# Performance work log

Hardware: AMD Instinct MI355X
Metric: run time of the kernel (lower is better)

## Reference

```python
import math
import jax, jax.numpy as jnp
import numpy as np

EMBED_DIM = 1024
NUM_HEADS = 16
HEAD_DIM = EMBED_DIM // NUM_HEADS


def setup_inputs() -> dict:
    key = jax.random.key(0)
    kx, kqkv, kproj = jax.random.split(key, 3)
    b, sq, h = 2, 2048, EMBED_DIM
    x = jax.random.normal(kx, (b, sq, h), dtype=jnp.float32)
    # torch Linear weights are [out_features, in_features]
    # xavier_uniform for qkv: bound = sqrt(6/(fan_in+fan_out))
    bound_qkv = math.sqrt(6.0 / (h + 3 * h))
    Wqkv = jax.random.uniform(kqkv, (3 * h, h), dtype=jnp.float32,
                              minval=-bound_qkv, maxval=bound_qkv)
    # kaiming_uniform(a=sqrt(5)) for proj: bound = 1/sqrt(fan_in)
    bound_p = 1.0 / math.sqrt(h)
    Wproj = jax.random.uniform(kproj, (h, h), dtype=jnp.float32,
                               minval=-bound_p, maxval=bound_p)
    bproj = jnp.zeros((h,), dtype=jnp.float32)
    # self-attention: query == key == value (module asserts equality)
    return {"query": x, "key": x, "value": x,
            "Wqkv": Wqkv, "Wproj": Wproj, "bproj": bproj}


def reference(query, key, value, Wqkv, Wproj, bproj):
    b, sq, h = query.shape
    nh, hn = NUM_HEADS, HEAD_DIM
    # permute to [sq, b, h] then flatten tokens (seq-major)
    x = jnp.transpose(query, (1, 0, 2)).reshape(sq * b, h)
    qkv = x @ Wqkv.T                       # [sq*b, 3h] (no qkv bias: add_bias_kv=False)
    qkv = qkv.reshape(sq, b, nh, 3 * hn)
    q, k, v = jnp.split(qkv, 3, axis=-1)   # each [sq, b, nh, hn]
    # view to (sq, b*nh, hn) then transpose(0,1) -> [b*nh, sq, hn] (b-major, nh-minor)
    q = q.reshape(sq, b * nh, hn).transpose(1, 0, 2)
    k = k.reshape(sq, b * nh, hn).transpose(1, 0, 2)
    v = v.reshape(sq, b * nh, hn).transpose(1, 0, 2)
    scale = 1.0 / math.sqrt(hn)
    scores = jnp.einsum('nqd,nkd->nqk', q, k) * scale   # [b*nh, sq, sq] full matrix
    attn = jax.nn.softmax(scores, axis=-1)
    ctx = jnp.einsum('nqk,nkd->nqd', attn, v)           # [b*nh, sq, hn]
    # NOTE: original code views the b*nh (b-major) dim as (nh, b) -- reproduce exactly
    ctx = ctx.reshape(nh, b, sq, hn)
    ctx = jnp.transpose(ctx, (2, 1, 0, 3)).reshape(sq * b, h)
    out = ctx @ Wproj.T + bproj
    out = out.reshape(sq, b, h)
    return jnp.transpose(out, (1, 0, 2))   # [b, sq, h]
```

## Files before the change

### kernel.cpp

```cpp
#include <hip/hip_runtime.h>
#include <stdint.h>

#define B_   2
#define SQ   2048
#define H    1024
#define NH   16
#define HN   64
#define T_TOK 4096
#define N3H  3072

typedef __bf16 bf16x8 __attribute__((ext_vector_type(8)));
typedef float  f32x4  __attribute__((ext_vector_type(4)));

#define MFMA16(a, b, c) __builtin_amdgcn_mfma_f32_16x16x32_bf16((a), (b), (c), 0, 0, 0)

#define LGKM_DRAIN() do { \
  __builtin_amdgcn_s_waitcnt(0xC07F); \
  __builtin_amdgcn_wave_barrier(); \
} while (0)

__device__ __forceinline__ uint16_t f2bf_u(float f) {
  union { float f; uint32_t u; } v; v.f = f;
  uint32_t u = v.u;
  u += 0x7fffu + ((u >> 16) & 1u);
  return (uint16_t)(u >> 16);
}

__device__ __forceinline__ bf16x8 ldb8(const uint16_t* p) {
  return *reinterpret_cast<const bf16x8*>(p);
}

__device__ __forceinline__ void gll16(const uint16_t* g, uint16_t* l) {
  __builtin_amdgcn_global_load_lds(
      (const __attribute__((address_space(1))) uint32_t*)g,
      (__attribute__((address_space(3))) uint32_t*)l, 16, 0, 0);
}

__global__ __launch_bounds__(256) void convert_kernel(
    const float* __restrict__ x, const float* __restrict__ wqkv,
    const float* __restrict__ wproj,
    uint16_t* __restrict__ xb, uint16_t* __restrict__ wqkvb,
    uint16_t* __restrict__ wprojb) {
  const int XT4 = (T_TOK * H) / 4;
  const int WQ4 = (N3H * H) / 4;
  int i4 = blockIdx.x * 256 + threadIdx.x;
  const float* src;
  uint16_t* dst;
  if (i4 < XT4) {
    int i = i4 * 4;
    int t = i >> 10, c = i & 1023;
    int bi = t & 1, s = t >> 1;
    src = x + (bi * SQ + s) * H + c;
    dst = xb + i;
  } else if (i4 < XT4 + WQ4) {
    int j = (i4 - XT4) * 4;
    src = wqkv + j; dst = wqkvb + j;
  } else {
    int j = (i4 - XT4 - WQ4) * 4;
    src = wproj + j; dst = wprojb + j;
  }
  float4 v = *(const float4*)src;
  ushort4 o;
  o.x = f2bf_u(v.x); o.y = f2bf_u(v.y); o.z = f2bf_u(v.z); o.w = f2bf_u(v.w);
  *(ushort4*)dst = o;
}

__global__ __launch_bounds__(256) void gemm_qkv_kernel(
    const uint16_t* __restrict__ xb, const uint16_t* __restrict__ wb,
    uint16_t* __restrict__ Qb, uint16_t* __restrict__ Kb,
    uint16_t* __restrict__ Vtb) {
  const int lane = threadIdx.x & 63;
  const int wave = threadIdx.x >> 6;
  const int quad = lane >> 4, l16 = lane & 15;
  const int wm = wave >> 1, wn = wave & 1;
  const int row0 = blockIdx.y * 128, col0 = blockIdx.x * 128;

  __shared__ __align__(16) char smem[4 * 64 * 76 * 2];
  uint16_t* sA = (uint16_t*)smem;
  uint16_t* sB = (uint16_t*)(smem + 8192);
  uint16_t* W  = (uint16_t*)(smem) + wave * (64 * 76);

  const int lrow = lane >> 2;
  const int lk   = (lane & 3) * 8;

  f32x4 acc[4][4];
#pragma unroll
  for (int i = 0; i < 4; ++i)
#pragma unroll
    for (int j = 0; j < 4; ++j) acc[i][j] = (f32x4){0.f, 0.f, 0.f, 0.f};

  for (int k0 = 0; k0 < H; k0 += 32) {
#pragma unroll
    for (int c = 0; c < 2; ++c) {
      int g = c * 4 + wave;
      gll16(xb + (size_t)(row0 + g * 16 + lrow) * H + k0 + lk, sA + g * 512);
      gll16(wb + (size_t)(col0 + g * 16 + lrow) * H + k0 + lk, sB + g * 512);
    }
    __syncthreads();
    bf16x8 af[4], bfr[4];
#pragma unroll
    for (int mt = 0; mt < 4; ++mt)
      af[mt] = ldb8(sA + (wm * 64 + mt * 16 + l16) * 32 + quad * 8);
#pragma unroll
    for (int nt = 0; nt < 4; ++nt)
      bfr[nt] = ldb8(sB + (wn * 64 + nt * 16 + l16) * 32 + quad * 8);
#pragma unroll
    for (int mt = 0; mt < 4; ++mt)
#pragma unroll
      for (int nt = 0; nt < 4; ++nt)
        acc[mt][nt] = MFMA16(af[mt], bfr[nt], acc[mt][nt]);
    __syncthreads();
  }

  const int c0 = col0 + wn * 64;
  const int cm = c0 >> 6;
  const int hd = cm / 3;
  const int which = cm - hd * 3;
  const int t0 = row0 + wm * 64;

  if (which < 2) {
#pragma unroll
    for (int mt = 0; mt < 4; ++mt)
#pragma unroll
      for (int nt = 0; nt < 4; ++nt)
#pragma unroll
        for (int r = 0; r < 4; ++r)
          W[(mt * 16 + quad * 4 + r) * 76 + nt * 16 + l16] = f2bf_u(acc[mt][nt][r]);
    LGKM_DRAIN();
    uint16_t* dstb = (which == 0) ? Qb : Kb;
    const int t8 = lane >> 3, d0 = (lane & 7) * 8;
#pragma unroll
    for (int it = 0; it < 8; ++it) {
      int tl = it * 8 + t8;
      int t = t0 + tl;
      int s = t >> 1;
      int n = (t & 1) * NH + hd;
      bf16x8 vv = ldb8(W + tl * 76 + d0);
      *(bf16x8*)(dstb + (size_t)(n * SQ + s) * HN + d0) = vv;
    }
  } else {
    uint32_t* W32 = (uint32_t*)W;
#pragma unroll
    for (int mt = 0; mt < 4; ++mt)
#pragma unroll
      for (int nt = 0; nt < 4; ++nt) {
        int base = (nt * 16 + l16) * 76 + mt * 8 + quad * 2;
        W32[base >> 1] =
            (uint32_t)f2bf_u(acc[mt][nt][0]) | ((uint32_t)f2bf_u(acc[mt][nt][2]) << 16);
        W32[(base >> 1) + 16] =
            (uint32_t)f2bf_u(acc[mt][nt][1]) | ((uint32_t)f2bf_u(acc[mt][nt][3]) << 16);
      }
    LGKM_DRAIN();
    const int dl = lane >> 3;
    const int bi = (lane >> 2) & 1;
    const int sc = (lane & 3) * 8;
    const int s0 = (row0 >> 1) + wm * 32;
    const int n = bi * NH + hd;
#pragma unroll
    for (int it = 0; it < 8; ++it) {
      int d = it * 8 + dl;
      bf16x8 vv = ldb8(W + d * 76 + bi * 32 + sc);
      *(bf16x8*)(Vtb + (size_t)(n * HN + d) * SQ + s0 + sc) = vv;
    }
  }
}

__global__ __launch_bounds__(512, 6) void attn_kernel(
    const uint16_t* __restrict__ Qb, const uint16_t* __restrict__ Kb,
    const uint16_t* __restrict__ Vtb, uint16_t* __restrict__ ctxb) {
  const int lane = threadIdx.x & 63;
  const int wave = threadIdx.x >> 6;
  const int quad = lane >> 4, l16 = lane & 15;
  const int head  = blockIdx.x;
  const int qtile = blockIdx.y;
  const int wq = wave & 3;
  const int hf = wave >> 2;
  const int q0 = qtile * 64 + wq * 16;

  const uint16_t* Qh = Qb + (size_t)head * SQ * HN;
  const uint16_t* Kh = Kb + (size_t)head * SQ * HN;
  const uint16_t* Vh = Vtb + (size_t)head * HN * SQ;

  __shared__ __align__(16) char smem_raw[51200];
  uint16_t (*stage)[2][64][64] = (uint16_t(*)[2][64][64])smem_raw;
  float (*cacc)[64][21]        = (float(*)[64][21])smem_raw;
  uint16_t (*plds)[16][72]     = (uint16_t(*)[16][72])(smem_raw + 32768);

  const int lr8 = lane >> 3;
  const int lc8 = lane & 7;
  const int sc8 = (lc8 - lr8) & 7;

  bf16x8 aq0 = ldb8(Qh + (q0 + l16) * HN + quad * 8);
  bf16x8 aq1 = ldb8(Qh + (q0 + l16) * HN + 32 + quad * 8);

  float lrun[4];
  f32x4 acc[4];
#pragma unroll
  for (int r = 0; r < 4; ++r) {
    lrun[r] = 0.f;
    acc[r] = (f32x4){0.f, 0.f, 0.f, 0.f};
  }
  const float sc2 = 0.125f * 1.44269504f;

  for (int kt = 0; kt < 16; ++kt) {
    const int kbase = (hf * 16 + kt) * 64;
#pragma unroll
    for (int j = 0; j < 2; ++j) {
      int rr = wq * 16 + j * 8;
      gll16(Kh + (size_t)(kbase + rr + lr8) * HN + sc8 * 8, &stage[hf][0][rr][0]);
      gll16(Vh + (size_t)(rr + lr8) * SQ + kbase + sc8 * 8, &stage[hf][1][rr][0]);
    }
    __syncthreads();

    f32x4 s4[4];
#pragma unroll
    for (int st = 0; st < 4; ++st) {
      bf16x8 k0 = ldb8(&stage[hf][0][st * 16 + l16][0] + ((quad + l16) & 7) * 8);
      bf16x8 k1 = ldb8(&stage[hf][0][st * 16 + l16][0] + ((quad + 4 + l16) & 7) * 8);
      f32x4 z = (f32x4){0.f, 0.f, 0.f, 0.f};
      z = MFMA16(aq0, k0, z);
      s4[st] = MFMA16(aq1, k1, z);
    }
#pragma unroll
    for (int st = 0; st < 4; ++st)
#pragma unroll
      for (int r = 0; r < 4; ++r) {
        float p = __builtin_amdgcn_exp2f(s4[st][r] * sc2);
        plds[wave][quad * 4 + r][st * 16 + l16] = f2bf_u(p);
        lrun[r] += p;
      }
    LGKM_DRAIN();
    bf16x8 ap0 = ldb8(&plds[wave][l16][quad * 8]);
    bf16x8 ap1 = ldb8(&plds[wave][l16][32 + quad * 8]);
#pragma unroll
    for (int dt = 0; dt < 4; ++dt) {
      bf16x8 v0 = ldb8(&stage[hf][1][dt * 16 + l16][0] + ((quad + l16) & 7) * 8);
      bf16x8 v1 = ldb8(&stage[hf][1][dt * 16 + l16][0] + ((quad + 4 + l16) & 7) * 8);
      acc[dt] = MFMA16(ap0, v0, acc[dt]);
      acc[dt] = MFMA16(ap1, v1, acc[dt]);
    }
    __syncthreads();
  }

  if (hf) {
    float* dst = cacc[wq][lane];
#pragma unroll
    for (int dt = 0; dt < 4; ++dt)
#pragma unroll
      for (int r = 0; r < 4; ++r) dst[dt * 4 + r] = acc[dt][r];
#pragma unroll
    for (int r = 0; r < 4; ++r) dst[16 + r] = lrun[r];
  }
  __syncthreads();
  if (hf) return;
  {
    const float* src = cacc[wq][lane];
#pragma unroll
    for (int dt = 0; dt < 4; ++dt)
#pragma unroll
      for (int r = 0; r < 4; ++r) acc[dt][r] += src[dt * 4 + r];
#pragma unroll
    for (int r = 0; r < 4; ++r) lrun[r] += src[16 + r];
  }

  float rinv[4];
#pragma unroll
  for (int r = 0; r < 4; ++r) {
    float ls = lrun[r];
    ls += __shfl_xor(ls, 1);
    ls += __shfl_xor(ls, 2);
    ls += __shfl_xor(ls, 4);
    ls += __shfl_xor(ls, 8);
    rinv[r] = __builtin_amdgcn_rcpf(ls);
  }
#pragma unroll
  for (int dt = 0; dt < 4; ++dt)
#pragma unroll
    for (int r = 0; r < 4; ++r)
      plds[wave][quad * 4 + r][dt * 16 + l16] = f2bf_u(acc[dt][r] * rinv[r]);
  LGKM_DRAIN();
  {
    const int q8 = lane >> 3, d0 = (lane & 7) * 8;
    const int gc = (head >> 1) * HN + d0;
#pragma unroll
    for (int it = 0; it < 2; ++it) {
      int ql = it * 8 + q8;
      bf16x8 vv = ldb8(&plds[wave][ql][d0]);
      int row = 2 * (q0 + ql) + (head & 1);
      *(bf16x8*)(ctxb + (size_t)row * H + gc) = vv;
    }
  }
}

__global__ __launch_bounds__(256) void gemm_proj_kernel(
    const uint16_t* __restrict__ ab, const uint16_t* __restrict__ wb,
    const float* __restrict__ bias, float* __restrict__ out) {
  const int lane = threadIdx.x & 63;
  const int wave = threadIdx.x >> 6;
  const int quad = lane >> 4, l16 = lane & 15;
  const int row0 = blockIdx.y * 128, col0 = blockIdx.x * 64;

  __shared__ __align__(16) uint16_t sA[128 * 32];
  __shared__ __align__(16) uint16_t sB[64 * 32];

  const int lrow = lane >> 2;
  const int lk   = (lane & 3) * 8;

  f32x4 acc[2][4];
#pragma unroll
  for (int i = 0; i < 2; ++i)
#pragma unroll
    for (int j = 0; j < 4; ++j) acc[i][j] = (f32x4){0.f, 0.f, 0.f, 0.f};

  for (int k0 = 0; k0 < H; k0 += 32) {
#pragma unroll
    for (int c = 0; c < 2; ++c) {
      int g = c * 4 + wave;
      gll16(ab + (size_t)(row0 + g * 16 + lrow) * H + k0 + lk, sA + g * 512);
    }
    gll16(wb + (size_t)(col0 + wave * 16 + lrow) * H + k0 + lk, sB + wave * 512);
    __syncthreads();
    bf16x8 af[2], bfr[4];
#pragma unroll
    for (int mt = 0; mt < 2; ++mt)
      af[mt] = ldb8(sA + (wave * 32 + mt * 16 + l16) * 32 + quad * 8);
#pragma unroll
    for (int nt = 0; nt < 4; ++nt)
      bfr[nt] = ldb8(sB + (nt * 16 + l16) * 32 + quad * 8);
#pragma unroll
    for (int mt = 0; mt < 2; ++mt)
#pragma unroll
      for (int nt = 0; nt < 4; ++nt)
        acc[mt][nt] = MFMA16(af[mt], bfr[nt], acc[mt][nt]);
    __syncthreads();
  }

#pragma unroll
  for (int mt = 0; mt < 2; ++mt)
#pragma unroll
    for (int nt = 0; nt < 4; ++nt)
#pragma unroll
      for (int r = 0; r < 4; ++r) {
        int m = row0 + wave * 32 + mt * 16 + quad * 4 + r;
        int c = col0 + nt * 16 + l16;
        int s = m >> 1, bi = m & 1;
        out[(size_t)(bi * SQ + s) * H + c] = acc[mt][nt][r] + bias[c];
      }
}

extern "C" void kernel_launch(void* const* d_in, const int* in_sizes, int n_in,
                              void* d_out, int out_size, void* d_ws, size_t ws_size,
                              hipStream_t stream) {
  const float* x     = (const float*)d_in[0];
  const float* wqkv  = (const float*)d_in[3];
  const float* wproj = (const float*)d_in[4];
  const float* bproj = (const float*)d_in[5];
  float* out = (float*)d_out;

  char* ws = (char*)d_ws;
  uint16_t* xb     = (uint16_t*)(ws);
  uint16_t* wqkvb  = (uint16_t*)(ws + (8ull  << 20));
  uint16_t* wprojb = (uint16_t*)(ws + (14ull << 20));
  uint16_t* Qb     = (uint16_t*)(ws + (16ull << 20));
  uint16_t* Kb     = (uint16_t*)(ws + (24ull << 20));
  uint16_t* Vtb    = (uint16_t*)(ws + (32ull << 20));
  uint16_t* ctxb   = (uint16_t*)(ws + (40ull << 20));

  convert_kernel<<<8192, 256, 0, stream>>>(x, wqkv, wproj, xb, wqkvb, wprojb);
  gemm_qkv_kernel<<<dim3(N3H / 128, T_TOK / 128), 256, 0, stream>>>(xb, wqkvb, Qb, Kb, Vtb);
  attn_kernel<<<dim3(B_ * NH, SQ / 64), 512, 0, stream>>>(Qb, Kb, Vtb, ctxb);
  gemm_proj_kernel<<<dim3(H / 64, T_TOK / 128), 256, 0, stream>>>(ctxb, wprojb, bproj, out);
}
```

Baseline: 227.4 us.

## Reuse K stage buffer for P tile to shrink attention LDS footprint

Drops the separate P scratch area in the attention kernel and writes the bf16 probability tile into the wave's own slice of the already-consumed K stage buffer, using an XOR-style swizzle. This cuts shared memory from 50 KB to 32 KB and raises the launch-bounds occupancy hint from 6 to 8, so more workgroups can reside per CU. In exchange it adds an extra block-wide barrier every key tile before P can overwrite K. The epilogue also now writes the context with scalar 2-byte global stores instead of staging through LDS for 16-byte stores, which risks poorly coalesced writes.

After: 302.0 us. 32.8% more time.

```diff
diff --git a/kernel.cpp b/kernel.cpp
--- a/kernel.cpp
+++ b/kernel.cpp
@@ -165,7 +165,7 @@
   }
 }
 
-__global__ __launch_bounds__(512, 6) void attn_kernel(
+__global__ __launch_bounds__(512, 8) void attn_kernel(
     const uint16_t* __restrict__ Qb, const uint16_t* __restrict__ Kb,
     const uint16_t* __restrict__ Vtb, uint16_t* __restrict__ ctxb) {
   const int lane = threadIdx.x & 63;
@@ -181,10 +181,10 @@
   const uint16_t* Kh = Kb + (size_t)head * SQ * HN;
   const uint16_t* Vh = Vtb + (size_t)head * HN * SQ;
 
-  __shared__ __align__(16) char smem_raw[51200];
+  __shared__ __align__(16) char smem_raw[32768];
   uint16_t (*stage)[2][64][64] = (uint16_t(*)[2][64][64])smem_raw;
   float (*cacc)[64][21]        = (float(*)[64][21])smem_raw;
-  uint16_t (*plds)[16][72]     = (uint16_t(*)[16][72])(smem_raw + 32768);
+  uint16_t* pz = &stage[hf][0][wq * 16][0];
 
   const int lr8 = lane >> 3;
   const int lc8 = lane & 7;
@@ -221,17 +221,21 @@
       z = MFMA16(aq0, k0, z);
       s4[st] = MFMA16(aq1, k1, z);
     }
+    __syncthreads();
+
 #pragma unroll
     for (int st = 0; st < 4; ++st)
 #pragma unroll
       for (int r = 0; r < 4; ++r) {
         float p = __builtin_amdgcn_exp2f(s4[st][r] * sc2);
-        plds[wave][quad * 4 + r][st * 16 + l16] = f2bf_u(p);
+        int row = quad * 4 + r;
+        int phys = (st * 2 + (l16 >> 3) + row) & 7;
+        pz[row * 64 + phys * 8 + (l16 & 7)] = f2bf_u(p);
         lrun[r] += p;
       }
     LGKM_DRAIN();
-    bf16x8 ap0 = ldb8(&plds[wave][l16][quad * 8]);
-    bf16x8 ap1 = ldb8(&plds[wave][l16][32 + quad * 8]);
+    bf16x8 ap0 = ldb8(pz + l16 * 64 + ((quad + l16) & 7) * 8);
+    bf16x8 ap1 = ldb8(pz + l16 * 64 + ((quad + 4 + l16) & 7) * 8);
 #pragma unroll
     for (int dt = 0; dt < 4; ++dt) {
       bf16x8 v0 = ldb8(&stage[hf][1][dt * 16 + l16][0] + ((quad + l16) & 7) * 8);
@@ -276,20 +280,14 @@
 #pragma unroll
   for (int dt = 0; dt < 4; ++dt)
 #pragma unroll
-    for (int r = 0; r < 4; ++r)
-      plds[wave][quad * 4 + r][dt * 16 + l16] = f2bf_u(acc[dt][r] * rinv[r]);
-  LGKM_DRAIN();
-  {
-    const int q8 = lane >> 3, d0 = (lane & 7) * 8;
-    const int gc = (head >> 1) * HN + d0;
-#pragma unroll
-    for (int it = 0; it < 2; ++it) {
-      int ql = it * 8 + q8;
-      bf16x8 vv = ldb8(&plds[wave][ql][d0]);
-      int row = 2 * (q0 + ql) + (head & 1);
-      *(bf16x8*)(ctxb + (size_t)row * H + gc) = vv;
-    }
-  }
+    for (int r = 0; r < 4; ++r) {
+      int qg = q0 + quad * 4 + r;
+      int dg = dt * 16 + l16;
+      float v = acc[dt][r] * rinv[r];
+      int row = qg * 2 + (head & 1);
+      int col = (head >> 1) * HN + dg;
+      ctxb[row * H + col] = f2bf_u(v);
+    }
 }
 
 __global__ __launch_bounds__(256) void gemm_proj_kernel(
```
